# Optimization experiments

Measured on AMD Instinct MI355X. Metric: run time of the kernel, lower is better.

## Reference

```python
import jax, jax.numpy as jnp
import numpy as np

N, E, R, C_IN, C_OUT = 100000, 1600000, 6, 8, 16
EPS = 1e-8


def setup_inputs() -> dict:
    key = jax.random.key(0)
    ks = jax.random.split(key, 6)
    x = jax.random.normal(ks[0], (N, C_IN), dtype=jnp.float32)
    supp_edges = jax.random.randint(ks[1], (E, 2), 0, N, dtype=jnp.int64)
    # (E, R, 2): real/imag of precomputed complex stencil (radial bins x transport x weights)
    lift_sten = jax.random.normal(ks[2], (E, R, 2), dtype=jnp.float32) * 0.1
    # TransField learned radial weights (real) and per-channel phase offsets (ftype=1)
    weight = jax.random.normal(ks[3], (R, C_IN, C_OUT), dtype=jnp.float32) * np.float32(1.0 / np.sqrt(R * C_IN))
    offset = jax.random.normal(ks[4], (C_IN, C_OUT), dtype=jnp.float32)
    # TangentNonLin per-channel magnitude bias (modReLU)
    bias = jax.random.normal(ks[5], (C_OUT,), dtype=jnp.float32) * 0.1
    return {"x": x, "supp_edges": supp_edges, "lift_sten": lift_sten,
            "weight": weight, "offset": offset, "bias": bias}


def reference(x, supp_edges, lift_sten, weight, offset, bias):
    src = supp_edges[:, 0]  # j: source
    dst = supp_edges[:, 1]  # i: target
    sten = jax.lax.complex(lift_sten[..., 0], lift_sten[..., 1])          # (E, R) complex64
    xj = x[src]                                                           # (E, Cin) gather
    # per-edge complex message over radial bins and input channels
    msg = sten[:, :, None] * xj[:, None, :].astype(sten.dtype)            # (E, R, Cin)
    agg = jax.ops.segment_sum(msg, dst, num_segments=N)                   # (N, R, Cin)
    # learned filter: real radial weights with per-channel phase offsets exp(i*theta)
    phase = jax.lax.complex(jnp.cos(offset), jnp.sin(offset))             # (Cin, Cout)
    filt = weight.astype(phase.dtype) * phase[None, :, :]                 # (R, Cin, Cout)
    y = jnp.einsum('nrc,rco->no', agg, filt)                              # (N, Cout) complex
    # TangentNonLin: modReLU on magnitude, phase preserved
    mag = jnp.abs(y)
    scale = jax.nn.relu(mag + bias[None, :]) / (mag + EPS)
    y = y * scale.astype(y.dtype)
    # return real/imag stacked for a real-valued output tensor (N, Cout, 2)
    return jnp.stack([jnp.real(y), jnp.imag(y)], axis=-1)
```

## Files before the change

### kernel.cpp

```cpp
#include <hip/hip_runtime.h>
#include <hip/hip_fp16.h>
#include <math.h>

#define N_NODES 100000
#define N_EDGES 1600000
#define RR      6
#define CIN     8
#define COUT    16
#define EPS     1e-8f

#define NBLK_A  512
#define ABLOCK  1024
#define CHUNK   (N_EDGES / NBLK_A)

#define NKEY    782
#define QCAP3   2304

#define LDS_SPAY   0
#define LDS_SHDR   75000
#define LDS_SBKT   87500
#define LDS_CNT    93752
#define LDS_TOTAL  106368

__device__ inline unsigned int pack_f16(float a, float b) {
    __half2 h = __floats2half2_rn(a, b);
    return *(unsigned int*)&h;
}

__global__ __launch_bounds__(ABLOCK)
void partition_kernel(const int* __restrict__ edges,
                      const float* __restrict__ sten,
                      int* __restrict__ gcur,
                      unsigned int* __restrict__ hdr,
                      unsigned int* __restrict__ pay) {
    extern __shared__ char smem[];
    uint2*          spay = (uint2*)(smem + LDS_SPAY);
    unsigned int*   shdr = (unsigned int*)(smem + LDS_SHDR);
    unsigned short* sbkt = (unsigned short*)(smem + LDS_SBKT);
    int* cnt   = (int*)(smem + LDS_CNT);
    int* cur   = cnt + NKEY;
    int* base  = cur + NKEY;
    int* gbase = base + NKEY;

    int tid = threadIdx.x;
    int blk = blockIdx.x;
    int e0 = blk * CHUNK;

    for (int i = tid; i < NKEY; i += ABLOCK) { cnt[i] = 0; cur[i] = 0; }
    __syncthreads();

    for (int i = tid; i < CHUNK; i += ABLOCK) {
        int2 ed = ((const int2*)edges)[e0 + i];
        atomicAdd(&cnt[ed.y >> 7], 1);
    }
    __syncthreads();

    if (tid < 64) {
        int lane = tid;
        int off = 0;
        for (int c = 0; c < NKEY; c += 64) {
            int idx = c + lane;
            int v = (idx < NKEY) ? cnt[idx] : 0;
            int orig = v;
#pragma unroll
            for (int d = 1; d < 64; d <<= 1) {
                int t = __shfl_up(v, d);
                if (lane >= d) v += t;
            }
            if (idx < NKEY) base[idx] = off + v - orig;
            off += __shfl(v, 63);
        }
    }
    __syncthreads();

    for (int b = tid; b < NKEY; b += ABLOCK) {
        int c = cnt[b];
        gbase[b] = (c > 0) ? atomicAdd(&gcur[b], c) : 0;
    }
    __syncthreads();

    for (int i = tid; i < CHUNK; i += ABLOCK) {
        int e = e0 + i;
        int2 ed = ((const int2*)edges)[e];
        int b = ed.y >> 7;
        int p = base[b] + atomicAdd(&cur[b], 1);
        sbkt[p] = (unsigned short)b;
        shdr[p] = ((unsigned int)ed.x << 8) | (unsigned int)(ed.y & 255);
        const float4* sp = (const float4*)(sten + (size_t)e * 12);
        float4 s0 = sp[0], s1 = sp[1], s2 = sp[2];
        uint2* dp = spay + p * 3;
        dp[0] = (uint2){ pack_f16(s0.x, s0.y), pack_f16(s0.z, s0.w) };
        dp[1] = (uint2){ pack_f16(s1.x, s1.y), pack_f16(s1.z, s1.w) };
        dp[2] = (uint2){ pack_f16(s2.x, s2.y), pack_f16(s2.z, s2.w) };
    }
    __syncthreads();

    for (int p = tid; p < CHUNK; p += ABLOCK) {
        int b = (int)sbkt[p];
        int rel = p - base[b];
        long long slot = (long long)gbase[b] + rel;
        if (slot < QCAP3) {
            size_t rs = (size_t)b * QCAP3 + slot;
            hdr[rs] = shdr[p];
            const uint2* sp = spay + p * 3;
            uint2 w0 = sp[0], w1 = sp[1], w2 = sp[2];
            unsigned int* dp = pay + rs * 6;
            *(uint2*)(dp + 0) = w0;
            *(uint2*)(dp + 2) = w1;
            *(uint2*)(dp + 4) = w2;
        }
    }
}

__global__ __launch_bounds__(512, 2)
void bucket_kernel(const float* __restrict__ x,
                   const float* __restrict__ weight,
                   const float* __restrict__ offset,
                   const float* __restrict__ bias,
                   const int* __restrict__ gcur,
                   const unsigned int* __restrict__ hdr,
                   const unsigned int* __restrict__ pay,
                   float* __restrict__ out) {
    __shared__ unsigned int idxs[QCAP3];
    __shared__ float fre[RR * CIN * COUT];
    __shared__ float fim[RR * CIN * COUT];
    __shared__ int cnt[128], nbase[128], cur2[128];
    __shared__ float bsh[COUT];
    __shared__ unsigned int perm[128];

    int tid = threadIdx.x;
    int key = blockIdx.x;

    for (int i = tid; i < RR * CIN * COUT; i += 512) {
        int co = i % (CIN * COUT);
        float w = weight[i], off = offset[co];
        fre[i] = w * cosf(off);
        fim[i] = w * sinf(off);
    }
    if (tid < COUT) bsh[tid] = bias[tid];
    if (tid < 128) { cnt[tid] = 0; cur2[tid] = 0; }
    __syncthreads();

    int T = gcur[key];
    if (T > QCAP3) T = QCAP3;

    const unsigned int* hslice = hdr + (size_t)key * QCAP3;
    const uint2* psrc = (const uint2*)(pay + (size_t)key * QCAP3 * 6);

    for (int i = tid; i < T * 3; i += 512) {
        uint2 v = psrc[i];
        asm volatile("" :: "v"(v.x), "v"(v.y));
    }

    for (int j = tid; j < T; j += 512) {
        unsigned int h = hslice[j];
        atomicAdd(&cnt[h & 127u], 1);
    }
    __syncthreads();

    if (tid < 128) {
        int lane = tid & 63;
        int half = tid >> 6;
        int v = cnt[tid];
        int orig = v;
#pragma unroll
        for (int d = 1; d < 64; d <<= 1) {
            int t = __shfl_up(v, d);
            if (lane >= d) v += t;
        }
        nbase[tid] = v - orig;
        if (lane == 63 && half == 0) cur2[127] = v;
    }
    __syncthreads();
    if (tid >= 64 && tid < 128) nbase[tid] += cur2[127];
    if (tid == 127) cur2[127] = 0;
    __syncthreads();

    for (int j = tid; j < T; j += 512) {
        unsigned int h = hslice[j];
        int d = (int)(h & 127u);
        int pos = nbase[d] + atomicAdd(&cur2[d], 1);
        idxs[pos] = ((h >> 8) << 12) | (unsigned int)j;
    }

    if (tid < 128) perm[tid] = ((unsigned int)cnt[tid] << 8) | (unsigned int)tid;
    __syncthreads();
    for (int k2 = 2; k2 <= 128; k2 <<= 1) {
        for (int jj = k2 >> 1; jj > 0; jj >>= 1) {
            if (tid < 128) {
                int ixj = tid ^ jj;
                if (ixj > tid) {
                    unsigned int a = perm[tid], c = perm[ixj];
                    bool up = ((tid & k2) == 0);
                    if (up ? (a > c) : (a < c)) { perm[tid] = c; perm[ixj] = a; }
                }
            }
            __syncthreads();
        }
    }

    int rank = tid >> 2;
    int l = tid & 3;
    unsigned int pk0 = perm[rank];
    int local = (int)(pk0 & 127u);
    int deg   = (int)(pk0 >> 8);
    int base  = nbase[local];
    int n = key * 128 + local;
    if (n >= N_NODES) return;

    float ar[RR][2] = {};
    float ai[RR][2] = {};

    uint2 p0 = {}, p1 = {}, p2 = {};
    float2 xv = {};
    if (deg > 0) {
        unsigned int pk = idxs[base];
        int j   = (int)(pk & 4095u);
        int src = (int)(pk >> 12);
        const uint2* pp = psrc + j * 3;
        p0 = pp[0]; p1 = pp[1]; p2 = pp[2];
        xv = *(const float2*)(x + (size_t)src * CIN + 2 * l);
    }
    for (int k = 0; k < deg; ++k) {
        uint2 q0 = {}, q1 = {}, q2 = {};
        float2 nx = {};
        if (k + 1 < deg) {
            unsigned int pk = idxs[base + k + 1];
            int j   = (int)(pk & 4095u);
            int src = (int)(pk >> 12);
            const uint2* pp = psrc + j * 3;
            q0 = pp[0]; q1 = pp[1]; q2 = pp[2];
            nx = *(const float2*)(x + (size_t)src * CIN + 2 * l);
        }
        unsigned int wv[6] = {p0.x, p0.y, p1.x, p1.y, p2.x, p2.y};
#pragma unroll
        for (int r = 0; r < RR; ++r) {
            __half2 hh = *(__half2*)&wv[r];
            float sre = __half2float(__low2half(hh));
            float sim = __half2float(__high2half(hh));
            ar[r][0] = fmaf(sre, xv.x, ar[r][0]);
            ar[r][1] = fmaf(sre, xv.y, ar[r][1]);
            ai[r][0] = fmaf(sim, xv.x, ai[r][0]);
            ai[r][1] = fmaf(sim, xv.y, ai[r][1]);
        }
        p0 = q0; p1 = q1; p2 = q2; xv = nx;
    }

    float yr[COUT], yi[COUT];
#pragma unroll
    for (int o = 0; o < COUT; ++o) { yr[o] = 0.f; yi[o] = 0.f; }
#pragma unroll
    for (int r = 0; r < RR; ++r) {
#pragma unroll
        for (int j = 0; j < 2; ++j) {
            int c = 2 * l + j;
            float are = ar[r][j], aim = ai[r][j];
            const float* fr = &fre[(r * CIN + c) * COUT];
            const float* fi = &fim[(r * CIN + c) * COUT];
#pragma unroll
            for (int o = 0; o < COUT; ++o) {
                yr[o] = fmaf(are, fr[o], yr[o]);
                yr[o] = fmaf(-aim, fi[o], yr[o]);
                yi[o] = fmaf(are, fi[o], yi[o]);
                yi[o] = fmaf(aim, fr[o], yi[o]);
            }
        }
    }
#pragma unroll
    for (int o = 0; o < COUT; ++o) {
        yr[o] += __shfl_xor(yr[o], 1);
        yr[o] += __shfl_xor(yr[o], 2);
        yi[o] += __shfl_xor(yi[o], 1);
        yi[o] += __shfl_xor(yi[o], 2);
    }
    float tmp[8];
    int ob = 4 * l;
#pragma unroll
    for (int j = 0; j < 4; ++j) {
        int o = ob + j;
        float re = yr[o], im = yi[o];
        float mag = sqrtf(re * re + im * im);
        float sc = fmaxf(mag + bsh[o], 0.f) / (mag + EPS);
        tmp[2 * j]     = re * sc;
        tmp[2 * j + 1] = im * sc;
    }
    float4* op = (float4*)(out + (size_t)n * 2 * COUT + 8 * l);
    op[0] = ((const float4*)tmp)[0];
    op[1] = ((const float4*)tmp)[1];
}

extern "C" void kernel_launch(void* const* d_in, const int* in_sizes, int n_in,
                              void* d_out, int out_size, void* d_ws, size_t ws_size,
                              hipStream_t stream) {
    const float* x      = (const float*)d_in[0];
    const int*   edges  = (const int*)d_in[1];
    const float* sten   = (const float*)d_in[2];
    const float* weight = (const float*)d_in[3];
    const float* offset = (const float*)d_in[4];
    const float* bias   = (const float*)d_in[5];
    float* out = (float*)d_out;

    int* gcur = (int*)d_ws;
    unsigned int* hdr = (unsigned int*)((char*)d_ws + 8192);
    unsigned int* pay = hdr + (size_t)NKEY * QCAP3;

    static int lds_inited = 0;
    if (!lds_inited) {
        (void)hipFuncSetAttribute((const void*)partition_kernel,
                                  hipFuncAttributeMaxDynamicSharedMemorySize,
                                  LDS_TOTAL);
        lds_inited = 1;
    }

    (void)hipMemsetAsync(gcur, 0, sizeof(int) * NKEY, stream);

    partition_kernel<<<NBLK_A, ABLOCK, LDS_TOTAL, stream>>>(edges, sten, gcur, hdr, pay);
    bucket_kernel<<<NKEY, 512, 0, stream>>>(x, weight, offset, bias,
                                            gcur, hdr, pay, out);
}
```

Baseline: 218.9 us.

## Split each node's edge list across two thread groups in bucket kernel

The bucket kernel now runs 1024 threads per block with 8 lanes per node instead of 4. Each half of a node's lanes walks half of its incoming edges, and the partial accumulators are then combined with a cross-lane shuffle. Each lane applies the filter for a single input channel, and the output reduction gains one more shuffle step. The goal is to shorten the serial per-node edge loop and expose more memory parallelism, at the cost of extra shuffles and larger blocks.

Result: slower. 274.2 us (+25.2%).

```diff
diff --git a/kernel.cpp b/kernel.cpp
--- a/kernel.cpp
+++ b/kernel.cpp
@@ -112,7 +112,7 @@
     }
 }
 
-__global__ __launch_bounds__(512, 2)
+__global__ __launch_bounds__(1024, 8)
 void bucket_kernel(const float* __restrict__ x,
                    const float* __restrict__ weight,
                    const float* __restrict__ offset,
@@ -131,7 +131,7 @@
     int tid = threadIdx.x;
     int key = blockIdx.x;
 
-    for (int i = tid; i < RR * CIN * COUT; i += 512) {
+    for (int i = tid; i < RR * CIN * COUT; i += 1024) {
         int co = i % (CIN * COUT);
         float w = weight[i], off = offset[co];
         fre[i] = w * cosf(off);
@@ -147,12 +147,12 @@
     const unsigned int* hslice = hdr + (size_t)key * QCAP3;
     const uint2* psrc = (const uint2*)(pay + (size_t)key * QCAP3 * 6);
 
-    for (int i = tid; i < T * 3; i += 512) {
+    for (int i = tid; i < T * 3; i += 1024) {
         uint2 v = psrc[i];
         asm volatile("" :: "v"(v.x), "v"(v.y));
     }
 
-    for (int j = tid; j < T; j += 512) {
+    for (int j = tid; j < T; j += 1024) {
         unsigned int h = hslice[j];
         atomicAdd(&cnt[h & 127u], 1);
     }
@@ -176,7 +176,7 @@
     if (tid == 127) cur2[127] = 0;
     __syncthreads();
 
-    for (int j = tid; j < T; j += 512) {
+    for (int j = tid; j < T; j += 1024) {
         unsigned int h = hslice[j];
         int d = (int)(h & 127u);
         int pos = nbase[d] + atomicAdd(&cur2[d], 1);
@@ -199,8 +199,10 @@
         }
     }
 
-    int rank = tid >> 2;
-    int l = tid & 3;
+    int s    = tid & 7;
+    int l    = s & 3;
+    int g    = s >> 2;
+    int rank = tid >> 3;
     unsigned int pk0 = perm[rank];
     int local = (int)(pk0 & 127u);
     int deg   = (int)(pk0 >> 8);
@@ -208,24 +210,28 @@
     int n = key * 128 + local;
     if (n >= N_NODES) return;
 
+    int degA   = (deg + 1) >> 1;
+    int mybase = base + g * degA;
+    int mydeg  = g ? (deg - degA) : degA;
+
     float ar[RR][2] = {};
     float ai[RR][2] = {};
 
     uint2 p0 = {}, p1 = {}, p2 = {};
     float2 xv = {};
-    if (deg > 0) {
-        unsigned int pk = idxs[base];
+    if (mydeg > 0) {
+        unsigned int pk = idxs[mybase];
         int j   = (int)(pk & 4095u);
         int src = (int)(pk >> 12);
         const uint2* pp = psrc + j * 3;
         p0 = pp[0]; p1 = pp[1]; p2 = pp[2];
         xv = *(const float2*)(x + (size_t)src * CIN + 2 * l);
     }
-    for (int k = 0; k < deg; ++k) {
+    for (int k = 0; k < mydeg; ++k) {
         uint2 q0 = {}, q1 = {}, q2 = {};
         float2 nx = {};
-        if (k + 1 < deg) {
-            unsigned int pk = idxs[base + k + 1];
+        if (k + 1 < mydeg) {
+            unsigned int pk = idxs[mybase + k + 1];
             int j   = (int)(pk & 4095u);
             int src = (int)(pk >> 12);
             const uint2* pp = psrc + j * 3;
@@ -246,47 +252,57 @@
         p0 = q0; p1 = q1; p2 = q2; xv = nx;
     }
 
+#pragma unroll
+    for (int r = 0; r < RR; ++r) {
+#pragma unroll
+        for (int j = 0; j < 2; ++j) {
+            ar[r][j] += __shfl_xor(ar[r][j], 4);
+            ai[r][j] += __shfl_xor(ai[r][j], 4);
+        }
+    }
+
+    int c = 2 * l + g;
+    float arc[RR], aic[RR];
+#pragma unroll
+    for (int r = 0; r < RR; ++r) { arc[r] = ar[r][g]; aic[r] = ai[r][g]; }
+
     float yr[COUT], yi[COUT];
 #pragma unroll
     for (int o = 0; o < COUT; ++o) { yr[o] = 0.f; yi[o] = 0.f; }
 #pragma unroll
     for (int r = 0; r < RR; ++r) {
-#pragma unroll
-        for (int j = 0; j < 2; ++j) {
-            int c = 2 * l + j;
-            float are = ar[r][j], aim = ai[r][j];
-            const float* fr = &fre[(r * CIN + c) * COUT];
-            const float* fi = &fim[(r * CIN + c) * COUT];
-#pragma unroll
-            for (int o = 0; o < COUT; ++o) {
-                yr[o] = fmaf(are, fr[o], yr[o]);
-                yr[o] = fmaf(-aim, fi[o], yr[o]);
-                yi[o] = fmaf(are, fi[o], yi[o]);
-                yi[o] = fmaf(aim, fr[o], yi[o]);
-            }
+        float are = arc[r], aim = aic[r];
+        const float* fr = &fre[(r * CIN + c) * COUT];
+        const float* fi = &fim[(r * CIN + c) * COUT];
+#pragma unroll
+        for (int o = 0; o < COUT; ++o) {
+            yr[o] = fmaf(are, fr[o], yr[o]);
+            yr[o] = fmaf(-aim, fi[o], yr[o]);
+            yi[o] = fmaf(are, fi[o], yi[o]);
+            yi[o] = fmaf(aim, fr[o], yi[o]);
         }
     }
 #pragma unroll
     for (int o = 0; o < COUT; ++o) {
         yr[o] += __shfl_xor(yr[o], 1);
         yr[o] += __shfl_xor(yr[o], 2);
+        yr[o] += __shfl_xor(yr[o], 4);
         yi[o] += __shfl_xor(yi[o], 1);
         yi[o] += __shfl_xor(yi[o], 2);
-    }
-    float tmp[8];
-    int ob = 4 * l;
-#pragma unroll
-    for (int j = 0; j < 4; ++j) {
-        int o = ob + j;
+        yi[o] += __shfl_xor(yi[o], 4);
+    }
+    float tmp[4];
+#pragma unroll
+    for (int j = 0; j < 2; ++j) {
+        int o = 2 * s + j;
         float re = yr[o], im = yi[o];
         float mag = sqrtf(re * re + im * im);
         float sc = fmaxf(mag + bsh[o], 0.f) / (mag + EPS);
         tmp[2 * j]     = re * sc;
         tmp[2 * j + 1] = im * sc;
     }
-    float4* op = (float4*)(out + (size_t)n * 2 * COUT + 8 * l);
+    float4* op = (float4*)(out + (size_t)n * 2 * COUT + 4 * s);
     op[0] = ((const float4*)tmp)[0];
-    op[1] = ((const float4*)tmp)[1];
 }
 
 extern "C" void kernel_launch(void* const* d_in, const int* in_sizes, int n_in,
@@ -315,6 +331,6 @@
     (void)hipMemsetAsync(gcur, 0, sizeof(int) * NKEY, stream);
 
     partition_kernel<<<NBLK_A, ABLOCK, LDS_TOTAL, stream>>>(edges, sten, gcur, hdr, pay);
-    bucket_kernel<<<NKEY, 512, 0, stream>>>(x, weight, offset, bias,
-                                            gcur, hdr, pay, out);
+    bucket_kernel<<<NKEY, 1024, 0, stream>>>(x, weight, offset, bias,
+                                             gcur, hdr, pay, out);
 }
```
